# Kernel optimization log

Hardware: AMD Instinct MI355X
Metric: run time of the kernel (lower is better)

Reference implementation:

```python
import jax, jax.numpy as jnp
import numpy as np

N = 1_000_000   # active voxels
CIN = 32
COUT = 64
K = 9           # 3x3 kernel offsets (rulebook size)
EPS = 1e-5


def setup_inputs() -> dict:
    key = jax.random.key(0)
    ks = jax.random.split(key, 6)
    x = jax.random.normal(ks[0], (N, CIN), dtype=jnp.float32)
    # rulebook: neighbor index per (voxel, kernel offset); stride=1 so same coord set
    nbr = jax.random.randint(ks[1], (N, K), 0, N, dtype=jnp.int32)
    W1 = jax.random.normal(ks[2], (K, CIN, COUT), dtype=jnp.float32) * (1.0 / np.sqrt(K * CIN))
    W2 = jax.random.normal(ks[3], (K, COUT, COUT), dtype=jnp.float32) * (1.0 / np.sqrt(K * COUT))
    Wd = jax.random.normal(ks[4], (CIN, COUT), dtype=jnp.float32) * (1.0 / np.sqrt(CIN))
    g1 = jnp.ones((COUT,), jnp.float32); b1 = jnp.zeros((COUT,), jnp.float32)
    g2 = jnp.ones((COUT,), jnp.float32); b2 = jnp.zeros((COUT,), jnp.float32)
    gd = jnp.ones((COUT,), jnp.float32); bd = jnp.zeros((COUT,), jnp.float32)
    return {"x": x, "W1": W1, "g1": g1, "b1": b1, "W2": W2, "g2": g2, "b2": b2,
            "Wd": Wd, "gd": gd, "bd": bd, "nbr": nbr}


def _sparse_conv(x, nbr, W):
    # gather-GEMM-scatter; loop over the fixed K=9 kernel offsets to avoid
    # materializing the full [N, K, Cin] gathered tensor
    out = jnp.zeros((x.shape[0], W.shape[-1]), dtype=x.dtype)
    for k in range(W.shape[0]):
        out = out + jnp.take(x, nbr[:, k], axis=0) @ W[k]
    return out


def _bn(x, gamma, beta):
    # BatchNorm1d over the voxel dimension (training-mode batch statistics)
    mu = jnp.mean(x, axis=0)
    var = jnp.var(x, axis=0)
    return gamma * (x - mu) * jax.lax.rsqrt(var + EPS) + beta


def reference(x, W1, g1, b1, W2, g2, b2, Wd, gd, bd, nbr):
    # downsample branch (1x1 conv -> BN, no relu) since in_ch != out_ch
    identity = _bn(x @ Wd, gd, bd)
    # conv1: SparseConv3x3 -> BN -> ReLU
    out = jax.nn.relu(_bn(_sparse_conv(x, nbr, W1), g1, b1))
    # conv2: SparseConv3x3 -> BN (no relu)
    out = _bn(_sparse_conv(out, nbr, W2), g2, b2)
    # residual add + final ReLU
    return jax.nn.relu(out + identity)
```

## Files before the change

### kernel.cpp

```cpp
#include <hip/hip_runtime.h>
#include <hip/hip_bf16.h>

#define NV 1000000
#define CI 32
#define CO 64
#define KK 9
#define NG (NV / 16)
#define EPSV 1e-5f

typedef __bf16 bf16x8 __attribute__((ext_vector_type(8)));
typedef float  f32x4  __attribute__((ext_vector_type(4)));

__device__ __forceinline__ f32x4 mfma16(bf16x8 a, bf16x8 b, f32x4 c) {
    return __builtin_amdgcn_mfma_f32_16x16x32_bf16(a, b, c, 0, 0, 0);
}

__device__ __forceinline__ float xredseg(float v) {
    v += __shfl_xor(v, 16, 64);
    v += __shfl_xor(v, 32, 64);
    return v;
}

__global__ void k_prep_w(const float* __restrict__ W1, const float* __restrict__ W2,
                         const float* __restrict__ Wd,
                         __bf16* __restrict__ W1T, __bf16* __restrict__ W2T,
                         __bf16* __restrict__ WdT) {
    int i = blockIdx.x * blockDim.x + threadIdx.x;
    const int n1 = KK * CO * CI;
    const int n2 = KK * CO * CO;
    const int nd = CO * CI;
    if (i < n1) {
        int k = i / (CO * CI), r = i % (CO * CI), co = r / CI, ci = r % CI;
        W1T[i] = (__bf16)W1[(k * CI + ci) * CO + co];
    } else if (i < n1 + n2) {
        int j = i - n1;
        int k = j / (CO * CO), r = j % (CO * CO), co = r / CO, ci = r % CO;
        W2T[j] = (__bf16)W2[(k * CO + ci) * CO + co];
    } else if (i < n1 + n2 + nd) {
        int j = i - n1 - n2;
        int co = j / CI, ci = j % CI;
        WdT[j] = (__bf16)Wd[ci * CO + co];
    }
}

__global__ void k_prep_x(const float* __restrict__ x, __bf16* __restrict__ xb) {
    int i = blockIdx.x * blockDim.x + threadIdx.x;
    const float4* px = (const float4*)x + 2 * (size_t)i;
    float4 u = px[0], v = px[1];
    bf16x8 o;
    o[0] = (__bf16)u.x; o[1] = (__bf16)u.y; o[2] = (__bf16)u.z; o[3] = (__bf16)u.w;
    o[4] = (__bf16)v.x; o[5] = (__bf16)v.y; o[6] = (__bf16)v.z; o[7] = (__bf16)v.w;
    *((bf16x8*)xb + i) = o;
}

__global__ __launch_bounds__(256, 2) void k_conv1(
    const __bf16* __restrict__ xb, const int* __restrict__ nbr,
    const __bf16* __restrict__ W1T, const __bf16* __restrict__ WdT,
    __bf16* __restrict__ y1b, float* __restrict__ stats) {
    __shared__ __align__(16) char w1smem[KK * CO * CI * 2];

    const int lane = threadIdx.x & 63;
    const int w    = threadIdx.x >> 6;
    const int r    = lane & 15;
    const int seg  = lane >> 4;

#pragma unroll
    for (int j = 0; j < 9; j++) {
        const __bf16* srcp = W1T + (size_t)(j * 256 + threadIdx.x) * 8;
        __builtin_amdgcn_global_load_lds(
            (const __attribute__((address_space(1))) void*)srcp,
            (__attribute__((address_space(3))) void*)(w1smem + j * 4096 + w * 1024),
            16, 0, 0);
    }
    __syncthreads();

    bf16x8 wd[4];
#pragma unroll
    for (int t = 0; t < 4; t++)
        wd[t] = *(const bf16x8*)(WdT + (size_t)(t * 16 + r) * CI + seg * 8);

    float ps1[4] = {0.f,0.f,0.f,0.f}, pq1[4] = {0.f,0.f,0.f,0.f};
    float psd[4] = {0.f,0.f,0.f,0.f}, pqd[4] = {0.f,0.f,0.f,0.f};

    const int slot   = blockIdx.x * 4 + w;
    const int stride = gridDim.x * 4;
    const f32x4 z = {0.f, 0.f, 0.f, 0.f};

    auto loadIdx = [&](int (&idx)[KK], int tile) {
        const int* nb = nbr + (size_t)(tile * 16 + r) * KK;
#pragma unroll
        for (int k = 0; k < KK; k++) idx[k] = nb[k];
    };
    auto gather9 = [&](bf16x8 (&g)[KK], const int (&idx)[KK]) {
#pragma unroll
        for (int k = 0; k < KK; k++)
            g[k] = *(const bf16x8*)(xb + (size_t)idx[k] * CI + seg * 8);
    };
    auto loadAd = [&](int tile) {
        return *(const bf16x8*)(xb + (size_t)(tile * 16 + r) * CI + seg * 8);
    };
    auto compute = [&](int tile, const bf16x8 (&g)[KK], bf16x8 ad) {
        int w1off = 0;
        asm volatile("" : "+v"(w1off));
        const __bf16* wb = (const __bf16*)w1smem + w1off;

        f32x4 acc[4]  = {z, z, z, z};
        f32x4 accd[4] = {z, z, z, z};
#pragma unroll
        for (int t = 0; t < 4; t++) accd[t] = mfma16(ad, wd[t], accd[t]);
#pragma unroll
        for (int k = 0; k < KK; k++) {
#pragma unroll
            for (int t = 0; t < 4; t++) {
                bf16x8 b = *(const bf16x8*)(wb + k * 2048 + t * 512 + r * 32 + seg * 8);
                acc[t] = mfma16(g[k], b, acc[t]);
            }
        }

        const int vb = tile * 16;
#pragma unroll
        for (int t = 0; t < 4; t++) {
#pragma unroll
            for (int rr = 0; rr < 4; rr++) {
                float val = acc[t][rr];
                int row = vb + seg * 4 + rr;
                __builtin_nontemporal_store((__bf16)val, &y1b[(size_t)row * CO + t * 16 + r]);
                ps1[t] += val; pq1[t] += val * val;
                float dv = accd[t][rr];
                psd[t] += dv; pqd[t] += dv * dv;
            }
        }
    };

    int idx0[KK], idx1[KK];
    bf16x8 g0[KK], g1[KK];
    bf16x8 ad0, ad1;

    int it = slot;
    loadIdx(idx0, it);
    gather9(g0, idx0); ad0 = loadAd(it);
    int itn = it + stride;
    bool have = (itn < NG);
    if (have) loadIdx(idx1, itn);

    while (true) {
        if (have) {
            gather9(g1, idx1); ad1 = loadAd(itn);
            int it2 = itn + stride;
            if (it2 < NG) loadIdx(idx0, it2);
        }
        compute(it, g0, ad0);
        if (!have) break;
        it = itn; itn = it + stride; have = (itn < NG);

        if (have) {
            gather9(g0, idx0); ad0 = loadAd(itn);
            int it2 = itn + stride;
            if (it2 < NG) loadIdx(idx1, it2);
        }
        compute(it, g1, ad1);
        if (!have) break;
        it = itn; itn = it + stride; have = (itn < NG);
    }

#pragma unroll
    for (int t = 0; t < 4; t++) {
        ps1[t] = xredseg(ps1[t]); pq1[t] = xredseg(pq1[t]);
        psd[t] = xredseg(psd[t]); pqd[t] = xredseg(pqd[t]);
    }
    if (lane < 16) {
#pragma unroll
        for (int t = 0; t < 4; t++) {
            atomicAdd(&stats[0 * 64 + t * 16 + lane], ps1[t]);
            atomicAdd(&stats[1 * 64 + t * 16 + lane], pq1[t]);
            atomicAdd(&stats[2 * 64 + t * 16 + lane], psd[t]);
            atomicAdd(&stats[3 * 64 + t * 16 + lane], pqd[t]);
        }
    }
}

#define TILE_B (16 * KK * 128)

__global__ __launch_bounds__(128, 2) void k_conv2(
    const __bf16* __restrict__ h1b, const int* __restrict__ nbr,
    const __bf16* __restrict__ W2T, const float* __restrict__ g1,
    const float* __restrict__ b1,
    float* __restrict__ y2, float* __restrict__ stats) {
    __shared__ __align__(16) char smem[2][TILE_B];

    const int lane = threadIdx.x & 63;
    const int w    = threadIdx.x >> 6;
    const int r    = lane & 15;
    const int seg  = lane >> 4;

    bf16x8 w2[KK][2][2];
#pragma unroll
    for (int k = 0; k < KK; k++)
#pragma unroll
        for (int t2 = 0; t2 < 2; t2++)
#pragma unroll
            for (int s = 0; s < 2; s++) {
                int co = w * 32 + t2 * 16 + r;
                int ci = s * 32 + seg * 8;
                w2[k][t2][s] = *(const bf16x8*)(W2T + ((size_t)(k * CO + co)) * CO + ci);
            }

    float scA[8], shA[8], scB[8], shB[8];
#pragma unroll
    for (int j = 0; j < 8; j++) {
        int cA = seg * 8 + j;
        float muA = stats[cA] * (1.0f / NV);
        float vaA = stats[64 + cA] * (1.0f / NV) - muA * muA;
        float sA  = g1[cA] * rsqrtf(vaA + EPSV);
        scA[j] = sA; shA[j] = b1[cA] - muA * sA;
        int cB = 32 + seg * 8 + j;
        float muB = stats[cB] * (1.0f / NV);
        float vaB = stats[64 + cB] * (1.0f / NV) - muB * muB;
        float sB  = g1[cB] * rsqrtf(vaB + EPSV);
        scB[j] = sB; shB[j] = b1[cB] - muB * sB;
    }

    float ps[2] = {0.f, 0.f}, pq[2] = {0.f, 0.f};
    const f32x4 z = {0.f, 0.f, 0.f, 0.f};
    const int sw = r & 7;

    auto stage = [&](char* buf, int it) {
        const int* nb = nbr + (size_t)it * (16 * KK);
#pragma unroll
        for (int s = 0; s < 9; s++) {
            int c = w * 576 + s * 64 + lane;
            int ruleIdx = c >> 3;
            int i = (ruleIdx * 57) >> 9;
            int p = (c & 7) ^ (i & 7);
            int idx = nb[ruleIdx];
            const __bf16* src = h1b + (size_t)idx * CO + p * 8;
            __builtin_amdgcn_global_load_lds(
                (const __attribute__((address_space(1))) void*)src,
                (__attribute__((address_space(3))) void*)(buf + w * 9216 + s * 1024),
                16, 0, 0);
        }
    };

    int it = blockIdx.x;
    int cur = 0;
    if (it < NG) stage(smem[0], it);
    __syncthreads();

    for (; it < NG; it += gridDim.x) {
        int nxt = it + gridDim.x;
        if (nxt < NG) stage(smem[cur ^ 1], nxt);

        const __bf16* base = (const __bf16*)smem[cur];
        f32x4 acc[2] = {z, z};
#pragma unroll
        for (int k = 0; k < KK; k++) {
            const __bf16* rp = base + (size_t)(r * KK + k) * 64;
            bf16x8 a0r = *(const bf16x8*)(rp + ((seg ^ sw) * 8));
            bf16x8 a1r = *(const bf16x8*)(rp + (((4 + seg) ^ sw) * 8));
            bf16x8 a0, a1;
#pragma unroll
            for (int j = 0; j < 8; j++) {
                a0[j] = (__bf16)fmaxf((float)a0r[j] * scA[j] + shA[j], 0.f);
                a1[j] = (__bf16)fmaxf((float)a1r[j] * scB[j] + shB[j], 0.f);
            }
            acc[0] = mfma16(a0, w2[k][0][0], acc[0]);
            acc[0] = mfma16(a1, w2[k][0][1], acc[0]);
            acc[1] = mfma16(a0, w2[k][1][0], acc[1]);
            acc[1] = mfma16(a1, w2[k][1][1], acc[1]);
        }

        const int vb = it * 16;
#pragma unroll
        for (int t2 = 0; t2 < 2; t2++) {
#pragma unroll
            for (int rr = 0; rr < 4; rr++) {
                float val = acc[t2][rr];
                int row = vb + seg * 4 + rr;
                int c = w * 32 + t2 * 16 + r;
                __builtin_nontemporal_store(val, &y2[(size_t)row * CO + c]);
                ps[t2] += val; pq[t2] += val * val;
            }
        }

        __syncthreads();
        cur ^= 1;
    }

#pragma unroll
    for (int t2 = 0; t2 < 2; t2++) { ps[t2] = xredseg(ps[t2]); pq[t2] = xredseg(pq[t2]); }
    if (lane < 16) {
#pragma unroll
        for (int t2 = 0; t2 < 2; t2++) {
            atomicAdd(&stats[4 * 64 + w * 32 + t2 * 16 + lane], ps[t2]);
            atomicAdd(&stats[5 * 64 + w * 32 + t2 * 16 + lane], pq[t2]);
        }
    }
}

__global__ __launch_bounds__(256, 2) void k_final(
    const __bf16* __restrict__ xb, const __bf16* __restrict__ WdT,
    float* __restrict__ out, const float* __restrict__ stats,
    const float* __restrict__ g2, const float* __restrict__ b2,
    const float* __restrict__ gd, const float* __restrict__ bd) {
    __shared__ float s2[CO], sh2[CO], sdv[CO], shd[CO];
    int t = threadIdx.x;
    if (t < CO) {
        float mu2  = stats[4 * 64 + t] * (1.0f / NV);
        float var2 = stats[5 * 64 + t] * (1.0f / NV) - mu2 * mu2;
        float s = g2[t] * rsqrtf(var2 + EPSV);
        s2[t] = s; sh2[t] = b2[t] - mu2 * s;
        float mud  = stats[2 * 64 + t] * (1.0f / NV);
        float vard = stats[3 * 64 + t] * (1.0f / NV) - mud * mud;
        float sd = gd[t] * rsqrtf(vard + EPSV);
        sdv[t] = sd; shd[t] = bd[t] - mud * sd;
    }
    __syncthreads();

    const int lane = threadIdx.x & 63;
    const int w    = threadIdx.x >> 6;
    const int r    = lane & 15;
    const int seg  = lane >> 4;

    bf16x8 wd[4];
#pragma unroll
    for (int t4 = 0; t4 < 4; t4++)
        wd[t4] = *(const bf16x8*)(WdT + (size_t)(t4 * 16 + r) * CI + seg * 8);

    const int slot = blockIdx.x * 4 + w;
    const int nslots = gridDim.x * 4;
    const f32x4 z = {0.f, 0.f, 0.f, 0.f};

    for (int gid = slot; gid < NG; gid += nslots) {
        const int vb = gid * 16;
        const int v  = vb + r;
        bf16x8 ad = *(const bf16x8*)(xb + (size_t)v * CI + seg * 8);
        f32x4 accd[4] = {z, z, z, z};
#pragma unroll
        for (int t4 = 0; t4 < 4; t4++) accd[t4] = mfma16(ad, wd[t4], accd[t4]);
#pragma unroll
        for (int t4 = 0; t4 < 4; t4++) {
#pragma unroll
            for (int rr = 0; rr < 4; rr++) {
                int row = vb + seg * 4 + rr;
                int c = t4 * 16 + r;
                size_t o = (size_t)row * CO + c;
                float y2v = out[o];
                float res = s2[c] * y2v + sh2[c] + sdv[c] * accd[t4][rr] + shd[c];
                out[o] = fmaxf(res, 0.f);
            }
        }
    }
}

extern "C" void kernel_launch(void* const* d_in, const int* in_sizes, int n_in,
                              void* d_out, int out_size, void* d_ws, size_t ws_size,
                              hipStream_t stream) {
    const float* x  = (const float*)d_in[0];
    const float* W1 = (const float*)d_in[1];
    const float* g1 = (const float*)d_in[2];
    const float* b1 = (const float*)d_in[3];
    const float* W2 = (const float*)d_in[4];
    const float* g2 = (const float*)d_in[5];
    const float* b2 = (const float*)d_in[6];
    const float* Wd = (const float*)d_in[7];
    const float* gd = (const float*)d_in[8];
    const float* bd = (const float*)d_in[9];
    const int*  nbr = (const int*)d_in[10];

    char* ws = (char*)d_ws;
    __bf16* xb  = (__bf16*)ws;
    __bf16* y1b = (__bf16*)(ws + 64000000);
    __bf16* W1T = (__bf16*)(ws + 192000000);
    __bf16* W2T = W1T + KK * CO * CI;
    __bf16* WdT = W2T + KK * CO * CO;
    float* stats = (float*)(ws + 192000000 + 2 * (KK*CO*CI + KK*CO*CO + CO*CI));

    hipMemsetAsync(stats, 0, 6 * 64 * sizeof(float), stream);

    int nprep = KK*CO*CI + KK*CO*CO + CO*CI;
    k_prep_w<<<(nprep + 255) / 256, 256, 0, stream>>>(W1, W2, Wd, W1T, W2T, WdT);
    k_prep_x<<<(NV * CI / 8) / 256, 256, 0, stream>>>(x, xb);
    k_conv1<<<768, 256, 0, stream>>>(xb, nbr, W1T, WdT, y1b, stats);
    k_conv2<<<1024, 128, 0, stream>>>(y1b, nbr, W2T, g1, b1, (float*)d_out, stats);
    k_final<<<1024, 256, 0, stream>>>(xb, WdT, (float*)d_out, stats, g2, b2, gd, bd);
}
```

Measured before the change: 601.8 us.

## Apply conv2 BN-ReLU once per gathered row via register-staged prefetch pipeline

In conv2, the gather of h1 rows moves from direct global-to-LDS loads to register loads, with neighbor indices and row data software-pipelined two tiles ahead. The BN1 scale/shift and ReLU are applied once per gathered 16-byte chunk before it is written to swizzled LDS, instead of on each A-operand read inside the MFMA loop. Each lane now needs only 8 channel coefficients instead of 32. This adds register pressure from holding 9 data vectors and 9 index sets in flight. The conv1 grid is also raised from 768 to 1024 blocks.

```diff
diff --git a/kernel.cpp b/kernel.cpp
--- a/kernel.cpp
+++ b/kernel.cpp
@@ -192,6 +192,7 @@
     const int w    = threadIdx.x >> 6;
     const int r    = lane & 15;
     const int seg  = lane >> 4;
+    const int p    = lane & 7;
 
     bf16x8 w2[KK][2][2];
 #pragma unroll
@@ -205,64 +206,72 @@
                 w2[k][t2][s] = *(const bf16x8*)(W2T + ((size_t)(k * CO + co)) * CO + ci);
             }
 
-    float scA[8], shA[8], scB[8], shB[8];
+    float scP[8], shP[8];
 #pragma unroll
     for (int j = 0; j < 8; j++) {
-        int cA = seg * 8 + j;
-        float muA = stats[cA] * (1.0f / NV);
-        float vaA = stats[64 + cA] * (1.0f / NV) - muA * muA;
-        float sA  = g1[cA] * rsqrtf(vaA + EPSV);
-        scA[j] = sA; shA[j] = b1[cA] - muA * sA;
-        int cB = 32 + seg * 8 + j;
-        float muB = stats[cB] * (1.0f / NV);
-        float vaB = stats[64 + cB] * (1.0f / NV) - muB * muB;
-        float sB  = g1[cB] * rsqrtf(vaB + EPSV);
-        scB[j] = sB; shB[j] = b1[cB] - muB * sB;
-    }
+        int c0 = p * 8 + j;
+        float mu  = stats[c0] * (1.0f / NV);
+        float var = stats[64 + c0] * (1.0f / NV) - mu * mu;
+        float s   = g1[c0] * rsqrtf(var + EPSV);
+        scP[j] = s; shP[j] = b1[c0] - mu * s;
+    }
+
+    int ri[9], dstoff[9];
+#pragma unroll
+    for (int s = 0; s < 9; s++) {
+        int c = w * 576 + s * 64 + lane;
+        int rIdx = c >> 3;
+        int i = (rIdx * 57) >> 9;
+        ri[s] = rIdx;
+        dstoff[s] = rIdx * 128 + ((p ^ (i & 7)) * 16);
+    }
+
+    auto loadIdx = [&](int (&ix)[9], int tile) {
+        const int* nb = nbr + (size_t)tile * (16 * KK);
+#pragma unroll
+        for (int s = 0; s < 9; s++) ix[s] = nb[ri[s]];
+    };
+    auto loadDat = [&](f32x4 (&d)[9], const int (&ix)[9]) {
+#pragma unroll
+        for (int s = 0; s < 9; s++)
+            d[s] = *(const f32x4*)(h1b + (size_t)ix[s] * CO + p * 8);
+    };
+    auto xform = [&](char* tb, const f32x4 (&d)[9]) {
+#pragma unroll
+        for (int s = 0; s < 9; s++) {
+            union { f32x4 f; bf16x8 b; } u; u.f = d[s];
+            bf16x8 o;
+#pragma unroll
+            for (int j = 0; j < 8; j++)
+                o[j] = (__bf16)fmaxf((float)u.b[j] * scP[j] + shP[j], 0.f);
+            *(bf16x8*)(tb + dstoff[s]) = o;
+        }
+    };
 
     float ps[2] = {0.f, 0.f}, pq[2] = {0.f, 0.f};
     const f32x4 z = {0.f, 0.f, 0.f, 0.f};
     const int sw = r & 7;
-
-    auto stage = [&](char* buf, int it) {
-        const int* nb = nbr + (size_t)it * (16 * KK);
-#pragma unroll
-        for (int s = 0; s < 9; s++) {
-            int c = w * 576 + s * 64 + lane;
-            int ruleIdx = c >> 3;
-            int i = (ruleIdx * 57) >> 9;
-            int p = (c & 7) ^ (i & 7);
-            int idx = nb[ruleIdx];
-            const __bf16* src = h1b + (size_t)idx * CO + p * 8;
-            __builtin_amdgcn_global_load_lds(
-                (const __attribute__((address_space(1))) void*)src,
-                (__attribute__((address_space(3))) void*)(buf + w * 9216 + s * 1024),
-                16, 0, 0);
-        }
-    };
-
+    const int G = gridDim.x;
+
+    int idxN[9]; f32x4 dat[9];
     int it = blockIdx.x;
+    loadIdx(idxN, it);
+    loadDat(dat, idxN);
+    { int t1 = it + G;     loadIdx(idxN, t1 < NG ? t1 : NG - 1); }
+    xform(smem[0], dat);
+    loadDat(dat, idxN);
+    { int t2 = it + 2 * G; loadIdx(idxN, t2 < NG ? t2 : NG - 1); }
+    __syncthreads();
     int cur = 0;
-    if (it < NG) stage(smem[0], it);
-    __syncthreads();
-
-    for (; it < NG; it += gridDim.x) {
-        int nxt = it + gridDim.x;
-        if (nxt < NG) stage(smem[cur ^ 1], nxt);
-
+
+    for (; it < NG; it += G) {
         const __bf16* base = (const __bf16*)smem[cur];
         f32x4 acc[2] = {z, z};
 #pragma unroll
         for (int k = 0; k < KK; k++) {
             const __bf16* rp = base + (size_t)(r * KK + k) * 64;
-            bf16x8 a0r = *(const bf16x8*)(rp + ((seg ^ sw) * 8));
-            bf16x8 a1r = *(const bf16x8*)(rp + (((4 + seg) ^ sw) * 8));
-            bf16x8 a0, a1;
-#pragma unroll
-            for (int j = 0; j < 8; j++) {
-                a0[j] = (__bf16)fmaxf((float)a0r[j] * scA[j] + shA[j], 0.f);
-                a1[j] = (__bf16)fmaxf((float)a1r[j] * scB[j] + shB[j], 0.f);
-            }
+            bf16x8 a0 = *(const bf16x8*)(rp + ((seg ^ sw) * 8));
+            bf16x8 a1 = *(const bf16x8*)(rp + (((4 + seg) ^ sw) * 8));
             acc[0] = mfma16(a0, w2[k][0][0], acc[0]);
             acc[0] = mfma16(a1, w2[k][0][1], acc[0]);
             acc[1] = mfma16(a0, w2[k][1][0], acc[1]);
@@ -282,8 +291,14 @@
             }
         }
 
-        __syncthreads();
-        cur ^= 1;
+        int nx = it + G;
+        if (nx < NG) {
+            xform(smem[cur ^ 1], dat);
+            loadDat(dat, idxN);
+            { int t3 = it + 3 * G; loadIdx(idxN, t3 < NG ? t3 : NG - 1); }
+            __syncthreads();
+            cur ^= 1;
+        }
     }
 
 #pragma unroll
@@ -380,7 +395,7 @@
     int nprep = KK*CO*CI + KK*CO*CO + CO*CI;
     k_prep_w<<<(nprep + 255) / 256, 256, 0, stream>>>(W1, W2, Wd, W1T, W2T, WdT);
     k_prep_x<<<(NV * CI / 8) / 256, 256, 0, stream>>>(x, xb);
-    k_conv1<<<768, 256, 0, stream>>>(xb, nbr, W1T, WdT, y1b, stats);
+    k_conv1<<<1024, 256, 0, stream>>>(xb, nbr, W1T, WdT, y1b, stats);
     k_conv2<<<1024, 128, 0, stream>>>(y1b, nbr, W2T, g1, b1, (float*)d_out, stats);
     k_final<<<1024, 256, 0, stream>>>(xb, WdT, (float*)d_out, stats, g2, b2, gd, bd);
 }
```

New measurement: 617.1 us. 2.5% more time.
